# Kernel tuning notes

Measured on AMD Instinct MI355X. Metric: run time of the kernel, lower is better.

Reference implementation:

```python
import jax, jax.numpy as jnp
import numpy as np


def _lstm(x, w_ih, w_hh, b_ih, b_hh):
    # x: [B, T, D]; w_ih: [4H, D]; w_hh: [4H, H]. PyTorch gate order: i, f, g, o.
    B, T, D = x.shape
    H = w_hh.shape[1]
    # Precompute input contributions for all timesteps: [B, T, 4H]
    xg = jnp.einsum('btd,gd->btg', x, w_ih) + b_ih + b_hh
    xg = jnp.transpose(xg, (1, 0, 2))  # [T, B, 4H]

    def step(carry, xt):
        h, c = carry
        gates = xt + h @ w_hh.T  # [B, 4H]
        i, f, g, o = jnp.split(gates, 4, axis=-1)
        i = jax.nn.sigmoid(i)
        f = jax.nn.sigmoid(f)
        g = jnp.tanh(g)
        o = jax.nn.sigmoid(o)
        c = f * c + i * g
        h = o * jnp.tanh(c)
        return (h, c), h

    h0 = jnp.zeros((B, H), dtype=x.dtype)
    c0 = jnp.zeros((B, H), dtype=x.dtype)
    (_, _), hs = jax.lax.scan(step, (h0, c0), xg)
    return jnp.transpose(hs, (1, 0, 2))  # [B, T, H]


def setup_inputs() -> dict:
    key = jax.random.key(0)
    ks = jax.random.split(key, 11)
    B, T, D, H1, H2, OUT = 2048, 128, 128, 128, 64, 64
    s1 = 1.0 / np.sqrt(H1)
    s2 = 1.0 / np.sqrt(H2)
    return {
        'x': jax.random.normal(ks[0], (B, T, D), dtype=jnp.float32),
        'w_ih1': jax.random.uniform(ks[1], (4 * H1, D), jnp.float32, -s1, s1),
        'w_hh1': jax.random.uniform(ks[2], (4 * H1, H1), jnp.float32, -s1, s1),
        'b_ih1': jax.random.uniform(ks[3], (4 * H1,), jnp.float32, -s1, s1),
        'b_hh1': jax.random.uniform(ks[4], (4 * H1,), jnp.float32, -s1, s1),
        'w_ih2': jax.random.uniform(ks[5], (4 * H2, H1), jnp.float32, -s2, s2),
        'w_hh2': jax.random.uniform(ks[6], (4 * H2, H2), jnp.float32, -s2, s2),
        'b_ih2': jax.random.uniform(ks[7], (4 * H2,), jnp.float32, -s2, s2),
        'b_hh2': jax.random.uniform(ks[8], (4 * H2,), jnp.float32, -s2, s2),
        'w_dense': jax.random.uniform(ks[9], (OUT, H2), jnp.float32, -s2, s2),
        'b_dense': jax.random.uniform(ks[10], (OUT,), jnp.float32, -s2, s2),
    }


def reference(x, w_ih1, w_hh1, b_ih1, b_hh1, w_ih2, w_hh2, b_ih2, b_hh2, w_dense, b_dense):
    # Dropout is identity in eval mode.
    h = _lstm(x, w_ih1, w_hh1, b_ih1, b_hh1)          # [B, T, H1]
    h = _lstm(h, w_ih2, w_hh2, b_ih2, b_hh2)          # [B, T, H2]
    last = h[:, -1, :]                                 # [B, H2]
    return jax.nn.relu(last @ w_dense.T + b_dense)     # [B, 64]
```

## Files before the change

### kernel.cpp

```cpp
#include <hip/hip_runtime.h>
#include <hip/hip_bf16.h>

#define BB  2048
#define TT  128
#define DD  128
#define HH1 128
#define GG1 512
#define HH2 64
#define GG2 256
#define OO  64

typedef __attribute__((ext_vector_type(8))) short  short8;
typedef __attribute__((ext_vector_type(4))) float  floatx4;

#define PIN(x) asm volatile("" : "+v"(x))

#define OFF_WHH1 0
#define OFF_WIH1 131072
#define OFF_WIH2 262144
#define OFF_WHH2 327680
#define OFF_B1   360448
#define OFF_B2   362496
#define OFF_XBF  524288
#define OFF_H1S  67633152

#define L2E      1.44269504088896340736f
#define TWO_L2E  2.88539008177792681472f

__device__ __forceinline__ short f2bf(float f) {
  unsigned u = __float_as_uint(f);
  unsigned r = (u + 0x7FFFu + ((u >> 16) & 1u)) >> 16;
  return (short)r;
}
__device__ __forceinline__ float exp2_f(float x) {
  float r; asm("v_exp_f32 %0, %1" : "=v"(r) : "v"(x)); return r;
}
__device__ __forceinline__ float sigm2(float y) {
  return __builtin_amdgcn_rcpf(1.0f + exp2_f(y));
}
__device__ __forceinline__ float tanh2(float y) {
  return fmaf(-2.0f, __builtin_amdgcn_rcpf(1.0f + exp2_f(y)), 1.0f);
}

__device__ __forceinline__ void lds_barrier() {
  asm volatile("s_waitcnt lgkmcnt(0)" ::: "memory");
  __builtin_amdgcn_s_barrier();
  asm volatile("" ::: "memory");
}

__global__ void k_prep(const float* __restrict__ wih1, const float* __restrict__ whh1,
                       const float* __restrict__ bih1, const float* __restrict__ bhh1,
                       const float* __restrict__ wih2, const float* __restrict__ whh2,
                       const float* __restrict__ bih2, const float* __restrict__ bhh2,
                       char* __restrict__ ws) {
  short* WHH1 = (short*)(ws + OFF_WHH1);
  short* WIH1 = (short*)(ws + OFF_WIH1);
  short* WIH2 = (short*)(ws + OFF_WIH2);
  short* WHH2 = (short*)(ws + OFF_WHH2);
  float* B1 = (float*)(ws + OFF_B1);
  float* B2 = (float*)(ws + OFF_B2);
  int idx = blockIdx.x * blockDim.x + threadIdx.x;
  int stride = gridDim.x * blockDim.x;
  const float SCI = -L2E, SCG = TWO_L2E;
  for (int i = idx; i < GG1 * DD; i += stride) {
    int g = (i >> 7) >> 7;
    float s = (g == 2) ? SCG : SCI;
    WIH1[i] = f2bf(wih1[i] * s); WHH1[i] = f2bf(whh1[i] * s);
  }
  for (int i = idx; i < GG2 * HH1; i += stride) {
    int g = (i >> 7) >> 6; float s = (g == 2) ? SCG : SCI;
    WIH2[i] = f2bf(wih2[i] * s);
  }
  for (int i = idx; i < GG2 * HH2; i += stride) {
    int g = (i >> 6) >> 6; float s = (g == 2) ? SCG : SCI;
    WHH2[i] = f2bf(whh2[i] * s);
  }
  for (int i = idx; i < GG1; i += stride) {
    float s = ((i >> 7) == 2) ? SCG : SCI;
    B1[i] = (bih1[i] + bhh1[i]) * s;
  }
  for (int i = idx; i < GG2; i += stride) {
    float s = ((i >> 6) == 2) ? SCG : SCI;
    B2[i] = (bih2[i] + bhh2[i]) * s;
  }
}

__global__ __launch_bounds__(256) void k_xcast(const float* __restrict__ x,
                                               short* __restrict__ xbf) {
  size_t i = ((size_t)blockIdx.x * 256 + threadIdx.x) * 8;
  float4 a = *(const float4*)&x[i];
  float4 b = *(const float4*)&x[i + 4];
  short8 o;
  o[0] = f2bf(a.x); o[1] = f2bf(a.y); o[2] = f2bf(a.z); o[3] = f2bf(a.w);
  o[4] = f2bf(b.x); o[5] = f2bf(b.y); o[6] = f2bf(b.z); o[7] = f2bf(b.w);
  *(short8*)&xbf[i] = o;
}

__global__ __launch_bounds__(512, 2) void k_rec1f(const char* __restrict__ ws,
                                                  short* __restrict__ h1s) {
  __shared__ short hbds[2][16 * 136];
  const short* WHH = (const short*)(ws + OFF_WHH1);
  const short* WIH = (const short*)(ws + OFF_WIH1);
  const short* XBF = (const short*)(ws + OFF_XBF);
  const float* B1 = (const float*)(ws + OFF_B1);
  const int lane = threadIdx.x & 63;
  const int wv = threadIdx.x >> 6;
  const int col = lane & 15, quad = lane >> 4;
  const int hc = wv * 16 + col;
  const int r0 = blockIdx.x * 8;

  short8 wh[4][4], wx[4][4];
#pragma unroll
  for (int gt = 0; gt < 4; ++gt)
#pragma unroll
    for (int kk = 0; kk < 4; ++kk) {
      wh[gt][kk] = *(const short8*)&WHH[(gt * 128 + hc) * HH1 + kk * 32 + quad * 8];
      wx[gt][kk] = *(const short8*)&WIH[(gt * 128 + hc) * DD + kk * 32 + quad * 8];
      PIN(wh[gt][kk]);
      PIN(wx[gt][kk]);
    }
  floatx4 BIASV[4];
#pragma unroll
  for (int gt = 0; gt < 4; ++gt) {
    float b = B1[gt * 128 + hc];
    BIASV[gt] = (floatx4){b, b, b, b};
    PIN(BIASV[gt]);
  }

  for (int i = threadIdx.x; i < 2 * 16 * 136; i += 512) ((short*)hbds)[i] = 0;

  const bool aload = (col < 8);
  const short* xbase = XBF + (size_t)(r0 + (col & 7)) * TT * DD;
  const short8 zz = {0, 0, 0, 0, 0, 0, 0, 0};
  short8 axA[4], axB[4];
  floatx4 accA[4], accB[4];

  {
    short8 ax0[4];
#pragma unroll
    for (int kk = 0; kk < 4; ++kk)
      ax0[kk] = aload ? *(const short8*)&xbase[kk * 32 + quad * 8] : zz;
#pragma unroll
    for (int gt = 0; gt < 4; ++gt)
      accA[gt] = __builtin_amdgcn_mfma_f32_16x16x32_bf16(ax0[0], wx[gt][0], BIASV[gt], 0, 0, 0);
#pragma unroll
    for (int kk = 1; kk < 4; ++kk)
#pragma unroll
      for (int gt = 0; gt < 4; ++gt)
        accA[gt] = __builtin_amdgcn_mfma_f32_16x16x32_bf16(ax0[kk], wx[gt][kk], accA[gt], 0, 0, 0);
  }
#pragma unroll
  for (int kk = 0; kk < 4; ++kk) {
    axA[kk] = aload ? *(const short8*)&xbase[DD + kk * 32 + quad * 8] : zz;
    axB[kk] = zz;
  }

  const int row0 = (quad & 1) * 4 + (quad >> 1) * 2;
  float c0 = 0.f, c1 = 0.f;
  __syncthreads();

  auto step = [&](int t, short* rbuf, short* wbuf, floatx4* A, floatx4* Bn,
                  short8* axC, short8* axP) {
    if (aload && t + 2 < TT) {
#pragma unroll
      for (int kk = 0; kk < 4; ++kk)
        axP[kk] = *(const short8*)&xbase[(t + 2) * DD + kk * 32 + quad * 8];
    }
    short8 ah[4];
#pragma unroll
    for (int kk = 0; kk < 4; ++kk)
      ah[kk] = *(const short8*)&rbuf[col * 136 + kk * 32 + quad * 8];
#pragma unroll
    for (int kk = 0; kk < 4; ++kk)
#pragma unroll
      for (int gt = 0; gt < 4; ++gt)
        A[gt] = __builtin_amdgcn_mfma_f32_16x16x32_bf16(ah[kk], wh[gt][kk], A[gt], 0, 0, 0);
#pragma unroll
    for (int gt = 0; gt < 4; ++gt)
      Bn[gt] = __builtin_amdgcn_mfma_f32_16x16x32_bf16(axC[0], wx[gt][0], BIASV[gt], 0, 0, 0);
#pragma unroll
    for (int kk = 1; kk < 4; ++kk)
#pragma unroll
      for (int gt = 0; gt < 4; ++gt)
        Bn[gt] = __builtin_amdgcn_mfma_f32_16x16x32_bf16(axC[kk], wx[gt][kk], Bn[gt], 0, 0, 0);

    float g0[4], g1[4];
#pragma unroll
    for (int gt = 0; gt < 4; ++gt) {
      float v2 = __shfl_xor(A[gt][2], 32);
      float v3 = __shfl_xor(A[gt][3], 32);
      g0[gt] = (quad < 2) ? A[gt][0] : v2;
      g1[gt] = (quad < 2) ? A[gt][1] : v3;
    }
    {
      float i0 = sigm2(g0[0]), f0 = sigm2(g0[1]), gg0 = tanh2(g0[2]), o0 = sigm2(g0[3]);
      c0 = fmaf(f0, c0, i0 * gg0);
      float hA = o0 * tanh2(c0 * TWO_L2E);
      float i1 = sigm2(g1[0]), f1 = sigm2(g1[1]), gg1 = tanh2(g1[2]), o1 = sigm2(g1[3]);
      c1 = fmaf(f1, c1, i1 * gg1);
      float hB = o1 * tanh2(c1 * TWO_L2E);
      short ha = f2bf(hA), hbv = f2bf(hB);
      wbuf[(row0)     * 136 + hc] = ha;
      wbuf[(row0 + 1) * 136 + hc] = hbv;
      h1s[((size_t)(r0 + row0)     * TT + t) * HH1 + hc] = ha;
      h1s[((size_t)(r0 + row0 + 1) * TT + t) * HH1 + hc] = hbv;
    }
    lds_barrier();
  };

  for (int t = 0; t < TT; t += 2) {
    step(t,     &hbds[0][0], &hbds[1][0], accA, accB, axA, axB);
    step(t + 1, &hbds[1][0], &hbds[0][0], accB, accA, axB, axA);
  }
}

__global__ __launch_bounds__(256, 2) void k_rec2r(const char* __restrict__ ws,
                                                  const short* __restrict__ h1s,
                                                  const float* __restrict__ wd,
                                                  const float* __restrict__ bd,
                                                  float* __restrict__ out) {
  __shared__ short hbds[2][16 * 72];
  __shared__ float h2f[4 * HH2];
  const short* WHH = (const short*)(ws + OFF_WHH2);
  const short* WIH = (const short*)(ws + OFF_WIH2);
  const float* B2 = (const float*)(ws + OFF_B2);
  const int lane = threadIdx.x & 63;
  const int wv = threadIdx.x >> 6;
  const int col = lane & 15, quad = lane >> 4;
  const int hc = wv * 16 + col;
  const int r0 = blockIdx.x * 4;

  short8 wh[4][2], wx[4][4];
#pragma unroll
  for (int gt = 0; gt < 4; ++gt) {
#pragma unroll
    for (int kk = 0; kk < 2; ++kk) {
      wh[gt][kk] = *(const short8*)&WHH[(gt * 64 + hc) * HH2 + kk * 32 + quad * 8];
      PIN(wh[gt][kk]);
    }
#pragma unroll
    for (int kk = 0; kk < 4; ++kk) {
      wx[gt][kk] = *(const short8*)&WIH[(gt * 64 + hc) * HH1 + kk * 32 + quad * 8];
      PIN(wx[gt][kk]);
    }
  }
  floatx4 BIASV[4];
#pragma unroll
  for (int gt = 0; gt < 4; ++gt) {
    float b = B2[gt * 64 + hc];
    BIASV[gt] = (floatx4){b, b, b, b};
    PIN(BIASV[gt]);
  }

  for (int i = threadIdx.x; i < 2 * 16 * 72; i += 256) ((short*)hbds)[i] = 0;

  const bool aload = (col < 4);
  const short* h1base = h1s + (size_t)(r0 + (col & 3)) * TT * HH1;
  const short8 zz = {0, 0, 0, 0, 0, 0, 0, 0};
  short8 axA[4], axB[4];
  floatx4 accA[4], accB[4];

  {
    short8 ax0[4];
#pragma unroll
    for (int kk = 0; kk < 4; ++kk)
      ax0[kk] = aload ? *(const short8*)&h1base[kk * 32 + quad * 8] : zz;
#pragma unroll
    for (int gt = 0; gt < 4; ++gt)
      accA[gt] = __builtin_amdgcn_mfma_f32_16x16x32_bf16(ax0[0], wx[gt][0], BIASV[gt], 0, 0, 0);
#pragma unroll
    for (int kk = 1; kk < 4; ++kk)
#pragma unroll
      for (int gt = 0; gt < 4; ++gt)
        accA[gt] = __builtin_amdgcn_mfma_f32_16x16x32_bf16(ax0[kk], wx[gt][kk], accA[gt], 0, 0, 0);
  }
#pragma unroll
  for (int kk = 0; kk < 4; ++kk) {
    axA[kk] = aload ? *(const short8*)&h1base[HH1 + kk * 32 + quad * 8] : zz;
    axB[kk] = zz;
  }

  const int row0 = (quad & 1) * 4 + (quad >> 1) * 2;
  const bool realq = ((quad & 1) == 0);
  float c0 = 0.f, c1 = 0.f;
  __syncthreads();

  auto step = [&](int t, short* rbuf, short* wbuf, floatx4* A, floatx4* Bn,
                  short8* axC, short8* axP) {
    if (aload && t + 2 < TT) {
#pragma unroll
      for (int kk = 0; kk < 4; ++kk)
        axP[kk] = *(const short8*)&h1base[(t + 2) * HH1 + kk * 32 + quad * 8];
    }
    short8 ah[2];
#pragma unroll
    for (int kk = 0; kk < 2; ++kk)
      ah[kk] = *(const short8*)&rbuf[col * 72 + kk * 32 + quad * 8];
#pragma unroll
    for (int kk = 0; kk < 2; ++kk)
#pragma unroll
      for (int gt = 0; gt < 4; ++gt)
        A[gt] = __builtin_amdgcn_mfma_f32_16x16x32_bf16(ah[kk], wh[gt][kk], A[gt], 0, 0, 0);
#pragma unroll
    for (int gt = 0; gt < 4; ++gt)
      Bn[gt] = __builtin_amdgcn_mfma_f32_16x16x32_bf16(axC[0], wx[gt][0], BIASV[gt], 0, 0, 0);
#pragma unroll
    for (int kk = 1; kk < 4; ++kk)
#pragma unroll
      for (int gt = 0; gt < 4; ++gt)
        Bn[gt] = __builtin_amdgcn_mfma_f32_16x16x32_bf16(axC[kk], wx[gt][kk], Bn[gt], 0, 0, 0);

    float g0[4], g1[4];
#pragma unroll
    for (int gt = 0; gt < 4; ++gt) {
      float v2 = __shfl_xor(A[gt][2], 32);
      float v3 = __shfl_xor(A[gt][3], 32);
      g0[gt] = (quad < 2) ? A[gt][0] : v2;
      g1[gt] = (quad < 2) ? A[gt][1] : v3;
    }
    {
      float i0 = sigm2(g0[0]), f0 = sigm2(g0[1]), gg0 = tanh2(g0[2]), o0 = sigm2(g0[3]);
      c0 = fmaf(f0, c0, i0 * gg0);
      float hA = o0 * tanh2(c0 * TWO_L2E);
      float i1 = sigm2(g1[0]), f1 = sigm2(g1[1]), gg1 = tanh2(g1[2]), o1 = sigm2(g1[3]);
      c1 = fmaf(f1, c1, i1 * gg1);
      float hB = o1 * tanh2(c1 * TWO_L2E);
      if (realq) {
        wbuf[(row0)     * 72 + hc] = f2bf(hA);
        wbuf[(row0 + 1) * 72 + hc] = f2bf(hB);
        if (t == TT - 1) {
          h2f[(row0)     * HH2 + hc] = hA;
          h2f[(row0 + 1) * HH2 + hc] = hB;
        }
      }
    }
    lds_barrier();
  };

  for (int t = 0; t < TT; t += 2) {
    step(t,     &hbds[0][0], &hbds[1][0], accA, accB, axA, axB);
    step(t + 1, &hbds[1][0], &hbds[0][0], accB, accA, axB, axA);
  }

  {
    const int o = threadIdx.x & 63;
    const int r = threadIdx.x >> 6;
    float acc = bd[o];
    for (int k = 0; k < HH2; ++k)
      acc = fmaf(h2f[r * HH2 + k], wd[o * HH2 + k], acc);
    out[(size_t)(r0 + r) * OO + o] = fmaxf(acc, 0.f);
  }
}

extern "C" void kernel_launch(void* const* d_in, const int* in_sizes, int n_in,
                              void* d_out, int out_size, void* d_ws, size_t ws_size,
                              hipStream_t stream) {
  const float* x       = (const float*)d_in[0];
  const float* w_ih1   = (const float*)d_in[1];
  const float* w_hh1   = (const float*)d_in[2];
  const float* b_ih1   = (const float*)d_in[3];
  const float* b_hh1   = (const float*)d_in[4];
  const float* w_ih2   = (const float*)d_in[5];
  const float* w_hh2   = (const float*)d_in[6];
  const float* b_ih2   = (const float*)d_in[7];
  const float* b_hh2   = (const float*)d_in[8];
  const float* w_dense = (const float*)d_in[9];
  const float* b_dense = (const float*)d_in[10];
  char* ws = (char*)d_ws;
  short* xbf = (short*)(ws + OFF_XBF);
  short* h1s = (short*)(ws + OFF_H1S);
  float* out = (float*)d_out;

  hipLaunchKernelGGL(k_prep, dim3(256), dim3(256), 0, stream,
                     w_ih1, w_hh1, b_ih1, b_hh1, w_ih2, w_hh2, b_ih2, b_hh2, ws);
  hipLaunchKernelGGL(k_xcast, dim3((BB * TT * DD) / (256 * 8)), dim3(256), 0, stream, x, xbf);
  hipLaunchKernelGGL(k_rec1f, dim3(BB / 8), dim3(512), 0, stream, ws, h1s);
  hipLaunchKernelGGL(k_rec2r, dim3(BB / 4), dim3(256), 0, stream, ws, h1s, w_dense, b_dense, out);
}
```

Baseline: 446.5 us.

## Warp-specialize layer-2 LSTM: producer waves compute input projection, consumer waves recur

Layer-2 recurrent kernel now uses 512-thread blocks handling 8 batch rows. Four waves compute the input-gate projection one step ahead and stage it in double-buffered LDS, while the other four run the hidden-state recurrence. The consumer waves seed their accumulators from LDS instead of recomputing the input MFMAs, which shortens the serial critical path per step. This costs extra LDS traffic and a shared barrier between the two wave groups every step, and rows 8-15 of each MFMA tile still compute padding.

```diff
diff --git a/kernel.cpp b/kernel.cpp
--- a/kernel.cpp
+++ b/kernel.cpp
@@ -214,133 +214,161 @@
   }
 }
 
-__global__ __launch_bounds__(256, 2) void k_rec2r(const char* __restrict__ ws,
+__global__ __launch_bounds__(512, 2) void k_rec2w(const char* __restrict__ ws,
                                                   const short* __restrict__ h1s,
                                                   const float* __restrict__ wd,
                                                   const float* __restrict__ bd,
                                                   float* __restrict__ out) {
-  __shared__ short hbds[2][16 * 72];
-  __shared__ float h2f[4 * HH2];
-  const short* WHH = (const short*)(ws + OFF_WHH2);
-  const short* WIH = (const short*)(ws + OFF_WIH2);
-  const float* B2 = (const float*)(ws + OFF_B2);
+  __shared__ __align__(16) float xacc[2][256 * 20];
+  __shared__ short hbuf[2][16 * 72];
+  __shared__ float h2f[8 * HH2];
   const int lane = threadIdx.x & 63;
   const int wv = threadIdx.x >> 6;
   const int col = lane & 15, quad = lane >> 4;
-  const int hc = wv * 16 + col;
-  const int r0 = blockIdx.x * 4;
-
-  short8 wh[4][2], wx[4][4];
-#pragma unroll
-  for (int gt = 0; gt < 4; ++gt) {
-#pragma unroll
-    for (int kk = 0; kk < 2; ++kk) {
-      wh[gt][kk] = *(const short8*)&WHH[(gt * 64 + hc) * HH2 + kk * 32 + quad * 8];
-      PIN(wh[gt][kk]);
+  const int r0 = blockIdx.x * 8;
+
+  for (int i = threadIdx.x; i < 2 * 256 * 20; i += 512) ((float*)xacc)[i] = 0.f;
+  for (int i = threadIdx.x; i < 2 * 16 * 72; i += 512) ((short*)hbuf)[i] = 0;
+
+  if (wv >= 4) {
+    const short* WIH = (const short*)(ws + OFF_WIH2);
+    const float* B2 = (const float*)(ws + OFF_B2);
+    const int hcp = (wv - 4) * 16 + col;
+    short8 wx[4][4];
+#pragma unroll
+    for (int gt = 0; gt < 4; ++gt)
+#pragma unroll
+      for (int kk = 0; kk < 4; ++kk) {
+        wx[gt][kk] = *(const short8*)&WIH[(gt * 64 + hcp) * HH1 + kk * 32 + quad * 8];
+        PIN(wx[gt][kk]);
+      }
+    floatx4 BIASV[4];
+#pragma unroll
+    for (int gt = 0; gt < 4; ++gt) {
+      float b = B2[gt * 64 + hcp];
+      BIASV[gt] = (floatx4){b, b, b, b};
+      PIN(BIASV[gt]);
+    }
+    const bool aload = (col < 8);
+    const short* h1base = h1s + (size_t)(r0 + (col & 7)) * TT * HH1;
+    const short8 zz = {0, 0, 0, 0, 0, 0, 0, 0};
+    short8 axA[4], axB[4];
+
+    {
+      short8 ax0[4];
+#pragma unroll
+      for (int kk = 0; kk < 4; ++kk)
+        ax0[kk] = aload ? *(const short8*)&h1base[kk * 32 + quad * 8] : zz;
+      floatx4 Bn[4];
+#pragma unroll
+      for (int gt = 0; gt < 4; ++gt)
+        Bn[gt] = __builtin_amdgcn_mfma_f32_16x16x32_bf16(ax0[0], wx[gt][0], BIASV[gt], 0, 0, 0);
+#pragma unroll
+      for (int kk = 1; kk < 4; ++kk)
+#pragma unroll
+        for (int gt = 0; gt < 4; ++gt)
+          Bn[gt] = __builtin_amdgcn_mfma_f32_16x16x32_bf16(ax0[kk], wx[gt][kk], Bn[gt], 0, 0, 0);
+      if (quad < 2) {
+#pragma unroll
+        for (int gt = 0; gt < 4; ++gt)
+          *(floatx4*)&xacc[0][(gt * 64 + hcp) * 20 + quad * 4] = Bn[gt];
+      }
     }
 #pragma unroll
     for (int kk = 0; kk < 4; ++kk) {
-      wx[gt][kk] = *(const short8*)&WIH[(gt * 64 + hc) * HH1 + kk * 32 + quad * 8];
-      PIN(wx[gt][kk]);
-    }
-  }
-  floatx4 BIASV[4];
-#pragma unroll
-  for (int gt = 0; gt < 4; ++gt) {
-    float b = B2[gt * 64 + hc];
-    BIASV[gt] = (floatx4){b, b, b, b};
-    PIN(BIASV[gt]);
-  }
-
-  for (int i = threadIdx.x; i < 2 * 16 * 72; i += 256) ((short*)hbds)[i] = 0;
-
-  const bool aload = (col < 4);
-  const short* h1base = h1s + (size_t)(r0 + (col & 3)) * TT * HH1;
-  const short8 zz = {0, 0, 0, 0, 0, 0, 0, 0};
-  short8 axA[4], axB[4];
-  floatx4 accA[4], accB[4];
-
-  {
-    short8 ax0[4];
-#pragma unroll
-    for (int kk = 0; kk < 4; ++kk)
-      ax0[kk] = aload ? *(const short8*)&h1base[kk * 32 + quad * 8] : zz;
+      axA[kk] = aload ? *(const short8*)&h1base[HH1 + kk * 32 + quad * 8] : zz;
+      axB[kk] = zz;
+    }
+    __syncthreads();
+
+    auto pstep = [&](int t, short8* axC, short8* axP) {
+      if (t + 1 < TT) {
+        floatx4 Bn[4];
+#pragma unroll
+        for (int gt = 0; gt < 4; ++gt)
+          Bn[gt] = __builtin_amdgcn_mfma_f32_16x16x32_bf16(axC[0], wx[gt][0], BIASV[gt], 0, 0, 0);
+#pragma unroll
+        for (int kk = 1; kk < 4; ++kk)
+#pragma unroll
+          for (int gt = 0; gt < 4; ++gt)
+            Bn[gt] = __builtin_amdgcn_mfma_f32_16x16x32_bf16(axC[kk], wx[gt][kk], Bn[gt], 0, 0, 0);
+        if (quad < 2) {
+#pragma unroll
+          for (int gt = 0; gt < 4; ++gt)
+            *(floatx4*)&xacc[(t + 1) & 1][(gt * 64 + hcp) * 20 + quad * 4] = Bn[gt];
+        }
+      }
+      if (aload && t + 2 < TT) {
+#pragma unroll
+        for (int kk = 0; kk < 4; ++kk)
+          axP[kk] = *(const short8*)&h1base[(t + 2) * HH1 + kk * 32 + quad * 8];
+      }
+      lds_barrier();
+    };
+
+    for (int t = 0; t < TT; t += 2) {
+      pstep(t, axA, axB);
+      pstep(t + 1, axB, axA);
+    }
+
+  } else {
+    const short* WHH = (const short*)(ws + OFF_WHH2);
+    const int hc = wv * 16 + col;
+    short8 wh[4][2];
 #pragma unroll
     for (int gt = 0; gt < 4; ++gt)
-      accA[gt] = __builtin_amdgcn_mfma_f32_16x16x32_bf16(ax0[0], wx[gt][0], BIASV[gt], 0, 0, 0);
-#pragma unroll
-    for (int kk = 1; kk < 4; ++kk)
+#pragma unroll
+      for (int kk = 0; kk < 2; ++kk) {
+        wh[gt][kk] = *(const short8*)&WHH[(gt * 64 + hc) * HH2 + kk * 32 + quad * 8];
+        PIN(wh[gt][kk]);
+      }
+    const int row0 = (quad & 1) * 4 + (quad >> 1) * 2;
+    float c0 = 0.f, c1 = 0.f;
+    __syncthreads();
+
+    auto cstep = [&](int t) {
+      const int cur = t & 1;
+      short8 ah[2];
+#pragma unroll
+      for (int kk = 0; kk < 2; ++kk)
+        ah[kk] = *(const short8*)&hbuf[cur][col * 72 + kk * 32 + quad * 8];
+      floatx4 A[4];
 #pragma unroll
       for (int gt = 0; gt < 4; ++gt)
-        accA[gt] = __builtin_amdgcn_mfma_f32_16x16x32_bf16(ax0[kk], wx[gt][kk], accA[gt], 0, 0, 0);
-  }
-#pragma unroll
-  for (int kk = 0; kk < 4; ++kk) {
-    axA[kk] = aload ? *(const short8*)&h1base[HH1 + kk * 32 + quad * 8] : zz;
-    axB[kk] = zz;
-  }
-
-  const int row0 = (quad & 1) * 4 + (quad >> 1) * 2;
-  const bool realq = ((quad & 1) == 0);
-  float c0 = 0.f, c1 = 0.f;
-  __syncthreads();
-
-  auto step = [&](int t, short* rbuf, short* wbuf, floatx4* A, floatx4* Bn,
-                  short8* axC, short8* axP) {
-    if (aload && t + 2 < TT) {
-#pragma unroll
-      for (int kk = 0; kk < 4; ++kk)
-        axP[kk] = *(const short8*)&h1base[(t + 2) * HH1 + kk * 32 + quad * 8];
-    }
-    short8 ah[2];
-#pragma unroll
-    for (int kk = 0; kk < 2; ++kk)
-      ah[kk] = *(const short8*)&rbuf[col * 72 + kk * 32 + quad * 8];
-#pragma unroll
-    for (int kk = 0; kk < 2; ++kk)
-#pragma unroll
-      for (int gt = 0; gt < 4; ++gt)
-        A[gt] = __builtin_amdgcn_mfma_f32_16x16x32_bf16(ah[kk], wh[gt][kk], A[gt], 0, 0, 0);
-#pragma unroll
-    for (int gt = 0; gt < 4; ++gt)
-      Bn[gt] = __builtin_amdgcn_mfma_f32_16x16x32_bf16(axC[0], wx[gt][0], BIASV[gt], 0, 0, 0);
-#pragma unroll
-    for (int kk = 1; kk < 4; ++kk)
-#pragma unroll
-      for (int gt = 0; gt < 4; ++gt)
-        Bn[gt] = __builtin_amdgcn_mfma_f32_16x16x32_bf16(axC[kk], wx[gt][kk], Bn[gt], 0, 0, 0);
-
-    float g0[4], g1[4];
-#pragma unroll
-    for (int gt = 0; gt < 4; ++gt) {
-      float v2 = __shfl_xor(A[gt][2], 32);
-      float v3 = __shfl_xor(A[gt][3], 32);
-      g0[gt] = (quad < 2) ? A[gt][0] : v2;
-      g1[gt] = (quad < 2) ? A[gt][1] : v3;
-    }
-    {
+        A[gt] = *(const floatx4*)&xacc[cur][(gt * 64 + hc) * 20 + quad * 4];
+#pragma unroll
+      for (int kk = 0; kk < 2; ++kk)
+#pragma unroll
+        for (int gt = 0; gt < 4; ++gt)
+          A[gt] = __builtin_amdgcn_mfma_f32_16x16x32_bf16(ah[kk], wh[gt][kk], A[gt], 0, 0, 0);
+
+      float g0[4], g1[4];
+#pragma unroll
+      for (int gt = 0; gt < 4; ++gt) {
+        float v2 = __shfl_xor(A[gt][2], 32);
+        float v3 = __shfl_xor(A[gt][3], 32);
+        g0[gt] = (quad < 2) ? A[gt][0] : v2;
+        g1[gt] = (quad < 2) ? A[gt][1] : v3;
+      }
       float i0 = sigm2(g0[0]), f0 = sigm2(g0[1]), gg0 = tanh2(g0[2]), o0 = sigm2(g0[3]);
       c0 = fmaf(f0, c0, i0 * gg0);
       float hA = o0 * tanh2(c0 * TWO_L2E);
       float i1 = sigm2(g1[0]), f1 = sigm2(g1[1]), gg1 = tanh2(g1[2]), o1 = sigm2(g1[3]);
       c1 = fmaf(f1, c1, i1 * gg1);
       float hB = o1 * tanh2(c1 * TWO_L2E);
-      if (realq) {
-        wbuf[(row0)     * 72 + hc] = f2bf(hA);
-        wbuf[(row0 + 1) * 72 + hc] = f2bf(hB);
-        if (t == TT - 1) {
-          h2f[(row0)     * HH2 + hc] = hA;
-          h2f[(row0 + 1) * HH2 + hc] = hB;
-        }
-      }
-    }
-    lds_barrier();
-  };
-
-  for (int t = 0; t < TT; t += 2) {
-    step(t,     &hbds[0][0], &hbds[1][0], accA, accB, axA, axB);
-    step(t + 1, &hbds[1][0], &hbds[0][0], accB, accA, axB, axA);
-  }
+      hbuf[cur ^ 1][(row0)     * 72 + hc] = f2bf(hA);
+      hbuf[cur ^ 1][(row0 + 1) * 72 + hc] = f2bf(hB);
+      if (t == TT - 1) {
+        h2f[(row0)     * HH2 + hc] = hA;
+        h2f[(row0 + 1) * HH2 + hc] = hB;
+      }
+      lds_barrier();
+    };
+
+    for (int t = 0; t < TT; ++t) cstep(t);
+  }
+
+  __syncthreads();
 
   {
     const int o = threadIdx.x & 63;
@@ -375,5 +403,5 @@
                      w_ih1, w_hh1, b_ih1, b_hh1, w_ih2, w_hh2, b_ih2, b_hh2, ws);
   hipLaunchKernelGGL(k_xcast, dim3((BB * TT * DD) / (256 * 8)), dim3(256), 0, stream, x, xbf);
   hipLaunchKernelGGL(k_rec1f, dim3(BB / 8), dim3(512), 0, stream, ws, h1s);
-  hipLaunchKernelGGL(k_rec2r, dim3(BB / 4), dim3(256), 0, stream, ws, h1s, w_dense, b_dense, out);
-}
+  hipLaunchKernelGGL(k_rec2w, dim3(BB / 8), dim3(512), 0, stream, ws, h1s, w_dense, b_dense, out);
+}
```

New measurement: 414.4 us. 1.08x faster.
